# Kernel tuning notes

Hardware: AMD Instinct MI355X
Metric: run time of the kernel (lower is better)

## Reference

```python
import jax, jax.numpy as jnp
import numpy as np

B, S, H, F, E, K = 2, 2048, 1024, 2048, 8, 2  # batch, seq, hidden, ffn, experts, top_k


def setup_inputs() -> dict:
    key = jax.random.key(0)
    k1, k2, k3, k4 = jax.random.split(key, 4)
    s = lambda n: 1.0 / np.sqrt(n)
    return {
        "x": jax.random.normal(k1, (B, S, H), jnp.float32),
        "w_router": jax.random.normal(k2, (H, E), jnp.float32) * s(H),
        "w_in": jax.random.normal(k3, (E, H, 2 * F), jnp.float32) * s(H),   # GLU: 2*ffn
        "w_out": jax.random.normal(k4, (E, F, H), jnp.float32) * s(F),
        "bias": jnp.zeros((H,), jnp.float32),
    }


def reference(x, w_router, w_in, w_out, bias):
    Bq, Sq, Hq = x.shape
    T = Bq * Sq
    xf = x.reshape(T, Hq)

    # --- TopKGating ---
    logits = xf @ w_router                       # [T, E]
    top_vals, top_idx = jax.lax.top_k(logits, K)  # [T, K]
    gates = jax.nn.softmax(top_vals, axis=-1)    # softmax over selected logits

    # JetMoE-style aux loss: switch loss + 0.1 * z-loss
    probs = jax.nn.softmax(logits, axis=-1)
    p = probs.sum(0); p = p / p.sum()
    freq = jnp.sum(jax.nn.one_hot(top_idx, E, dtype=logits.dtype), axis=(0, 1))
    f = freq / freq.sum()
    lsesq = jnp.sum(jax.nn.logsumexp(logits, axis=-1) ** 2)
    loss = E * jnp.sum(p * f) + 0.1 * lsesq / T

    # --- dispatch: one row per (token, selected expert) pair, token-major ---
    eid = top_idx.reshape(-1)                    # [T*K] expert id per row
    g = gates.reshape(-1)                        # [T*K] gate per row
    tok = jnp.repeat(jnp.arange(T), K)           # [T*K] source token per row
    xr = jnp.repeat(xf, K, axis=0)               # [T*K, H]

    # --- grouped expert GEMMs (masked per-expert; math-equivalent to grouped GEMM) ---
    out_rows = jnp.zeros((T * K, Hq), x.dtype)
    for e in range(E):
        sel = (eid == e).astype(x.dtype)[:, None]
        h = (xr * sel) @ w_in[e]                 # [T*K, 2F]
        a, gv = jnp.split(h, 2, axis=-1)
        h = jax.nn.silu(a) * gv                  # GLU
        out_rows = out_rows + sel * (h @ w_out[e])

    # --- combine: scale by gates, scatter-add back to tokens ---
    out_rows = out_rows * g[:, None]
    y = jax.ops.segment_sum(out_rows, tok, num_segments=T)
    y = y.reshape(Bq, Sq, Hq) + bias
    return y, loss
```

## Files before the change

kernel.cpp:

```cpp
#include <hip/hip_runtime.h>
#include <hip/hip_bf16.h>
#include <math.h>

#define T_TOK 4096
#define HDIM  1024
#define FDIM  2048
#define EDIM  8
#define KSEL  2
#define TKROW 8192
#define N2F   4096
#define MAX_SLOTS 72

typedef __attribute__((ext_vector_type(8))) short short8;
typedef __attribute__((ext_vector_type(4))) float f32x4;

__device__ __forceinline__ unsigned short f32_to_bf16(float f) {
  unsigned int u = __float_as_uint(f);
  u += 0x7FFFu + ((u >> 16) & 1u);
  return (unsigned short)(u >> 16);
}

__device__ __forceinline__ void gload16(const void* g, void* l) {
  __builtin_amdgcn_global_load_lds(
      (const __attribute__((address_space(1))) unsigned int*)g,
      (__attribute__((address_space(3))) unsigned int*)l, 16, 0, 0);
}


__global__ void conv_x_kernel(const float* __restrict__ x,
                              unsigned short* __restrict__ xb, int n) {
  int i = (blockIdx.x * blockDim.x + threadIdx.x) * 4;
  if (i < n) {
    float4 v = *(const float4*)(x + i);
    ushort4 o;
    o.x = f32_to_bf16(v.x); o.y = f32_to_bf16(v.y);
    o.z = f32_to_bf16(v.z); o.w = f32_to_bf16(v.w);
    *(ushort4*)(xb + i) = o;
  }
}

__global__ void transpose_conv_kernel(const float* __restrict__ in,
                                      unsigned short* __restrict__ out,
                                      int R, int C) {
  __shared__ float tile[64][65];
  long base = (long)blockIdx.z * (long)R * (long)C;
  int c0 = blockIdx.x * 64, r0 = blockIdx.y * 64;
  int tx = threadIdx.x & 63;
  int ty = threadIdx.x >> 6;
  #pragma unroll
  for (int j = 0; j < 64; j += 4) {
    int r = r0 + ty + j;
    tile[ty + j][tx] = in[base + (long)r * C + c0 + tx];
  }
  __syncthreads();
  #pragma unroll
  for (int j = 0; j < 64; j += 4) {
    int oc = ty + j;
    out[base + (long)(c0 + oc) * R + r0 + tx] = f32_to_bf16(tile[tx][oc]);
  }
}

__global__ void router_kernel(const float* __restrict__ x,
                              const float* __restrict__ wr,
                              int* __restrict__ eid, float* __restrict__ tgate,
                              float* __restrict__ p_sum,
                              float* __restrict__ lse2_sum,
                              int* __restrict__ counts) {
  __shared__ float s_p[EDIM];
  __shared__ float s_lse2;
  __shared__ int s_cnt[EDIM];
  if (threadIdx.x < EDIM) { s_p[threadIdx.x] = 0.f; s_cnt[threadIdx.x] = 0; }
  if (threadIdx.x == 0) s_lse2 = 0.f;
  __syncthreads();

  int wave = threadIdx.x >> 6;
  int lane = threadIdx.x & 63;

  for (int it = 0; it < 4; ++it) {
    int t = (blockIdx.x * 4 + wave) + it * 1024;
    float acc[EDIM];
    #pragma unroll
    for (int e = 0; e < EDIM; e++) acc[e] = 0.f;
    const float* xr = x + (long)t * HDIM;
    for (int h = lane; h < HDIM; h += 64) {
      float xv = xr[h];
      const float* w = wr + h * EDIM;
      #pragma unroll
      for (int e = 0; e < EDIM; e++) acc[e] += xv * w[e];
    }
    #pragma unroll
    for (int e = 0; e < EDIM; e++) {
      float v = acc[e];
      for (int off = 32; off > 0; off >>= 1) v += __shfl_down(v, off);
      acc[e] = v;
    }
    if (lane == 0) {
      float m = acc[0];
      #pragma unroll
      for (int e = 1; e < EDIM; e++) m = fmaxf(m, acc[e]);
      float ex[EDIM]; float se = 0.f;
      #pragma unroll
      for (int e = 0; e < EDIM; e++) { ex[e] = __expf(acc[e] - m); se += ex[e]; }
      float lse = m + __logf(se);
      atomicAdd(&s_lse2, lse * lse);
      float inv = 1.f / se;
      #pragma unroll
      for (int e = 0; e < EDIM; e++) atomicAdd(&s_p[e], ex[e] * inv);
      int i1 = 0;
      #pragma unroll
      for (int e = 1; e < EDIM; e++) if (acc[e] > acc[i1]) i1 = e;
      int i2 = (i1 == 0) ? 1 : 0;
      #pragma unroll
      for (int e = 0; e < EDIM; e++) if (e != i1 && acc[e] > acc[i2]) i2 = e;
      float g1 = 1.f / (1.f + __expf(acc[i2] - acc[i1]));
      eid[t * 2] = i1; eid[t * 2 + 1] = i2;
      tgate[t * 2] = g1; tgate[t * 2 + 1] = 1.f - g1;
      atomicAdd(&s_cnt[i1], 1); atomicAdd(&s_cnt[i2], 1);
    }
  }
  __syncthreads();
  if (threadIdx.x < EDIM) {
    atomicAdd(&p_sum[threadIdx.x], s_p[threadIdx.x]);
    atomicAdd(&counts[threadIdx.x], s_cnt[threadIdx.x]);
  }
  if (threadIdx.x == 0) atomicAdd(lse2_sum, s_lse2);
}

__global__ void scan_kernel(const int* __restrict__ counts,
                            int* __restrict__ offsets, int* __restrict__ slot_e,
                            int* __restrict__ slot_m0, int* __restrict__ slot_rows,
                            int* __restrict__ n_slots, int* __restrict__ cursors) {
  int off = 0, s = 0;
  for (int e = 0; e < EDIM; e++) {
    offsets[e] = off;
    cursors[e] = 0;
    int c = counts[e];
    for (int m0 = 0; m0 < c; m0 += 128) {
      slot_e[s] = e; slot_m0[s] = off + m0;
      slot_rows[s] = min(128, c - m0); s++;
    }
    off += c;
  }
  *n_slots = s;
}

__global__ void scatter_kernel(const int* __restrict__ eid,
                               const float* __restrict__ tgate,
                               const int* __restrict__ offsets,
                               int* __restrict__ cursors,
                               int* __restrict__ btok, float* __restrict__ bgate,
                               int* __restrict__ tpos) {
  __shared__ int lcnt[EDIM];
  __shared__ int lbase[EDIM];
  int tid = threadIdx.x;
  if (tid < EDIM) lcnt[tid] = 0;
  __syncthreads();
  int t = blockIdx.x * 256 + tid;
  int e0 = eid[t * 2], e1 = eid[t * 2 + 1];
  int p0 = atomicAdd(&lcnt[e0], 1);
  int p1 = atomicAdd(&lcnt[e1], 1);
  __syncthreads();
  if (tid < EDIM) lbase[tid] = atomicAdd(&cursors[tid], lcnt[tid]);
  __syncthreads();
  int r0 = offsets[e0] + lbase[e0] + p0;
  int r1 = offsets[e1] + lbase[e1] + p1;
  btok[r0] = t; bgate[r0] = tgate[t * 2];     tpos[t * 2] = r0;
  btok[r1] = t; bgate[r1] = tgate[t * 2 + 1]; tpos[t * 2 + 1] = r1;
}

__global__ __launch_bounds__(256) void gemm1_kernel(
    const unsigned short* __restrict__ xb,
    const unsigned short* __restrict__ w_inT,
    const int* __restrict__ btok,
    const int* __restrict__ slot_e, const int* __restrict__ slot_m0,
    const int* __restrict__ slot_rows, const int* __restrict__ n_slots,
    unsigned short* __restrict__ glu)
{
  int bx = blockIdx.x;
  int slot = (bx & 7) * 9 + (bx >> 3);
  if (slot >= *n_slots) return;
  int e = slot_e[slot], r0 = slot_m0[slot], nrows = slot_rows[slot];
  int by = blockIdx.y;

  __shared__ unsigned short lA[128 * 64];
  __shared__ unsigned short lB[128 * 64];

  int tid = threadIdx.x;
  int lane = tid & 63, wv = tid >> 6;
  int wr = wv >> 1, wc = wv & 1;
  int lm = lane & 15, lq = lane >> 4, l7 = lane & 7;

  int srow = tid >> 3, skc = tid & 7;
  const unsigned short* asrc[4];
  const unsigned short* bsrc[4];
  #pragma unroll
  for (int i = 0; i < 4; ++i) {
    int row = srow + i * 32;
    int swz = (skc ^ (row & 7)) * 8;
    int ar = min(row, nrows - 1);
    int tok = btok[r0 + ar];
    asrc[i] = xb + (long)tok * HDIM + swz;
    int group = row >> 5, within = row & 31;
    int bcol = by * 64 + (group >> 1) * 32 + within + ((group & 1) ? FDIM : 0);
    bsrc[i] = w_inT + ((long)e * N2F + bcol) * HDIM + swz;
  }
  unsigned short* adst = lA + tid * 8;
  unsigned short* bdst = lB + tid * 8;

  f32x4 acc[4][4];
  #pragma unroll
  for (int mf = 0; mf < 4; ++mf)
    #pragma unroll
    for (int nf = 0; nf < 4; ++nf) acc[mf][nf] = (f32x4){0.f, 0.f, 0.f, 0.f};

  for (int k0 = 0; k0 < HDIM; k0 += 64) {
    #pragma unroll
    for (int i = 0; i < 4; ++i) {
      gload16(asrc[i] + k0, adst + i * 2048);
      gload16(bsrc[i] + k0, bdst + i * 2048);
    }
    __syncthreads();
    #pragma unroll
    for (int ks = 0; ks < 2; ++ks) {
      short8 a[4], b[4];
      #pragma unroll
      for (int mf = 0; mf < 4; ++mf) {
        int row = wr * 64 + mf * 16 + lm;
        a[mf] = *(const short8*)&lA[row * 64 + (((ks * 4 + lq) ^ l7) * 8)];
      }
      #pragma unroll
      for (int nf = 0; nf < 4; ++nf) {
        int n = wc * 64 + nf * 16 + lm;
        b[nf] = *(const short8*)&lB[n * 64 + (((ks * 4 + lq) ^ l7) * 8)];
      }
      #pragma unroll
      for (int mf = 0; mf < 4; ++mf)
        #pragma unroll
        for (int nf = 0; nf < 4; ++nf)
          acc[mf][nf] = __builtin_amdgcn_mfma_f32_16x16x32_bf16(a[mf], b[nf], acc[mf][nf], 0, 0, 0);
    }
    __syncthreads();
  }

  #pragma unroll
  for (int mf = 0; mf < 4; ++mf) {
    #pragma unroll
    for (int r = 0; r < 4; ++r) {
      int row = wr * 64 + mf * 16 + lq * 4 + r;
      if (row < nrows) {
        #pragma unroll
        for (int nf = 0; nf < 2; ++nf) {
          float a = acc[mf][nf][r];
          float g = acc[mf][nf + 2][r];
          float val = (a / (1.f + __expf(-a))) * g;
          glu[(long)(r0 + row) * FDIM + by * 64 + wc * 32 + nf * 16 + lm] = f32_to_bf16(val);
        }
      }
    }
  }
}

__global__ __launch_bounds__(256) void gemm2_kernel(
    const unsigned short* __restrict__ glu,
    const unsigned short* __restrict__ w_outT,
    const float* __restrict__ bgate,
    const int* __restrict__ slot_e, const int* __restrict__ slot_m0,
    const int* __restrict__ slot_rows, const int* __restrict__ n_slots,
    float* __restrict__ orows)
{
  int bx = blockIdx.x;
  int slot = (bx & 7) * 9 + (bx >> 3);
  if (slot >= *n_slots) return;
  int e = slot_e[slot], r0 = slot_m0[slot], nrows = slot_rows[slot];
  int c0 = blockIdx.y * 128;

  __shared__ unsigned short lA[128 * 64];
  __shared__ unsigned short lB[128 * 64];

  int tid = threadIdx.x;
  int lane = tid & 63, wv = tid >> 6;
  int wr = wv >> 1, wc = wv & 1;
  int lm = lane & 15, lq = lane >> 4, l7 = lane & 7;

  int srow = tid >> 3, skc = tid & 7;
  const unsigned short* asrc[4];
  const unsigned short* bsrc[4];
  #pragma unroll
  for (int i = 0; i < 4; ++i) {
    int row = srow + i * 32;
    int swz = (skc ^ (row & 7)) * 8;
    int ar = min(row, nrows - 1);
    asrc[i] = glu + (long)(r0 + ar) * FDIM + swz;
    bsrc[i] = w_outT + ((long)e * HDIM + c0 + row) * FDIM + swz;
  }
  unsigned short* adst = lA + tid * 8;
  unsigned short* bdst = lB + tid * 8;

  f32x4 acc[4][4];
  #pragma unroll
  for (int mf = 0; mf < 4; ++mf)
    #pragma unroll
    for (int nf = 0; nf < 4; ++nf) acc[mf][nf] = (f32x4){0.f, 0.f, 0.f, 0.f};

  for (int k0 = 0; k0 < FDIM; k0 += 64) {
    #pragma unroll
    for (int i = 0; i < 4; ++i) {
      gload16(asrc[i] + k0, adst + i * 2048);
      gload16(bsrc[i] + k0, bdst + i * 2048);
    }
    __syncthreads();
    #pragma unroll
    for (int ks = 0; ks < 2; ++ks) {
      short8 a[4], b[4];
      #pragma unroll
      for (int mf = 0; mf < 4; ++mf) {
        int row = wr * 64 + mf * 16 + lm;
        a[mf] = *(const short8*)&lA[row * 64 + (((ks * 4 + lq) ^ l7) * 8)];
      }
      #pragma unroll
      for (int nf = 0; nf < 4; ++nf) {
        int n = wc * 64 + nf * 16 + lm;
        b[nf] = *(const short8*)&lB[n * 64 + (((ks * 4 + lq) ^ l7) * 8)];
      }
      #pragma unroll
      for (int mf = 0; mf < 4; ++mf)
        #pragma unroll
        for (int nf = 0; nf < 4; ++nf)
          acc[mf][nf] = __builtin_amdgcn_mfma_f32_16x16x32_bf16(a[mf], b[nf], acc[mf][nf], 0, 0, 0);
    }
    __syncthreads();
  }

  #pragma unroll
  for (int mf = 0; mf < 4; ++mf) {
    #pragma unroll
    for (int r = 0; r < 4; ++r) {
      int row = wr * 64 + mf * 16 + lq * 4 + r;
      if (row < nrows) {
        float g = bgate[r0 + row];
        #pragma unroll
        for (int nf = 0; nf < 4; ++nf) {
          orows[(long)(r0 + row) * HDIM + c0 + wc * 64 + nf * 16 + lm] = acc[mf][nf][r] * g;
        }
      }
    }
  }
}

__global__ void combine_kernel(const float* __restrict__ orows,
                               const int* __restrict__ tpos,
                               const float* __restrict__ bias,
                               float* __restrict__ y) {
  int i = blockIdx.x * 256 + threadIdx.x;
  int t = i >> 8;
  int h = (i & 255) * 4;
  int p0 = tpos[t * 2], p1 = tpos[t * 2 + 1];
  float4 a = *(const float4*)(orows + (long)p0 * HDIM + h);
  float4 b = *(const float4*)(orows + (long)p1 * HDIM + h);
  float4 bv = *(const float4*)(bias + h);
  float4 o;
  o.x = a.x + b.x + bv.x; o.y = a.y + b.y + bv.y;
  o.z = a.z + b.z + bv.z; o.w = a.w + b.w + bv.w;
  *(float4*)(y + (long)t * HDIM + h) = o;
}

__global__ void finalize_kernel(const float* __restrict__ p_sum,
                                const float* __restrict__ lse2,
                                const int* __restrict__ counts,
                                float* __restrict__ loss_out) {
  float P = 0.f;
  for (int e = 0; e < EDIM; e++) P += p_sum[e];
  float dot = 0.f;
  for (int e = 0; e < EDIM; e++)
    dot += (p_sum[e] / P) * ((float)counts[e] / (float)TKROW);
  *loss_out = (float)EDIM * dot + 0.1f * (*lse2) / (float)T_TOK;
}

extern "C" void kernel_launch(void* const* d_in, const int* in_sizes, int n_in,
                              void* d_out, int out_size, void* d_ws, size_t ws_size,
                              hipStream_t stream) {
  const float* x        = (const float*)d_in[0];
  const float* w_router = (const float*)d_in[1];
  const float* w_in     = (const float*)d_in[2];
  const float* w_out    = (const float*)d_in[3];
  const float* bias     = (const float*)d_in[4];
  float* y = (float*)d_out;

  char* ws = (char*)d_ws;
  size_t o = 0;
  auto alloc = [&](size_t bytes) { size_t r = o; o = (o + bytes + 255) & ~(size_t)255; return r; };
  size_t o_meta    = alloc(256);
  size_t o_offsets = alloc(EDIM * 4);
  size_t o_slot_e  = alloc(MAX_SLOTS * 4);
  size_t o_slot_m0 = alloc(MAX_SLOTS * 4);
  size_t o_slot_nr = alloc(MAX_SLOTS * 4);
  size_t o_eid     = alloc((size_t)T_TOK * 2 * 4);
  size_t o_tgate   = alloc((size_t)T_TOK * 2 * 4);
  size_t o_tpos    = alloc((size_t)T_TOK * 2 * 4);
  size_t o_btok    = alloc((size_t)TKROW * 4);
  size_t o_bgate   = alloc((size_t)TKROW * 4);
  size_t o_xb      = alloc((size_t)T_TOK * HDIM * 2);
  size_t o_winT    = alloc((size_t)EDIM * N2F * HDIM * 2);
  size_t o_woutT   = alloc((size_t)EDIM * HDIM * FDIM * 2);
  size_t o_glu     = alloc((size_t)TKROW * FDIM * 2);
  size_t o_orows   = o_winT;
  (void)ws_size;

  float* p_sum   = (float*)(ws + o_meta);
  float* lse2    = (float*)(ws + o_meta + 32);
  int*   counts  = (int*)(ws + o_meta + 64);
  int*   cursors = (int*)(ws + o_meta + 96);
  int*   n_slots = (int*)(ws + o_meta + 128);
  int*   offsets = (int*)(ws + o_offsets);
  int*   slot_e  = (int*)(ws + o_slot_e);
  int*   slot_m0 = (int*)(ws + o_slot_m0);
  int*   slot_nr = (int*)(ws + o_slot_nr);
  int*   eid     = (int*)(ws + o_eid);
  float* tgate   = (float*)(ws + o_tgate);
  int*   tpos    = (int*)(ws + o_tpos);
  int*   btok    = (int*)(ws + o_btok);
  float* bgate   = (float*)(ws + o_bgate);
  unsigned short* xb    = (unsigned short*)(ws + o_xb);
  unsigned short* winT  = (unsigned short*)(ws + o_winT);
  unsigned short* woutT = (unsigned short*)(ws + o_woutT);
  unsigned short* glu   = (unsigned short*)(ws + o_glu);
  float* orows = (float*)(ws + o_orows);

  hipMemsetAsync(ws, 0, 256, stream);

  conv_x_kernel<<<dim3((T_TOK * HDIM) / 1024), dim3(256), 0, stream>>>(
      x, xb, T_TOK * HDIM);
  transpose_conv_kernel<<<dim3(N2F / 64, HDIM / 64, EDIM), dim3(256), 0, stream>>>(
      w_in, winT, HDIM, N2F);
  transpose_conv_kernel<<<dim3(HDIM / 64, FDIM / 64, EDIM), dim3(256), 0, stream>>>(
      w_out, woutT, FDIM, HDIM);

  router_kernel<<<dim3(256), dim3(256), 0, stream>>>(
      x, w_router, eid, tgate, p_sum, lse2, counts);
  scan_kernel<<<dim3(1), dim3(1), 0, stream>>>(
      counts, offsets, slot_e, slot_m0, slot_nr, n_slots, cursors);
  scatter_kernel<<<dim3(T_TOK / 256), dim3(256), 0, stream>>>(
      eid, tgate, offsets, cursors, btok, bgate, tpos);

  gemm1_kernel<<<dim3(MAX_SLOTS, FDIM / 64), dim3(256), 0, stream>>>(
      xb, winT, btok, slot_e, slot_m0, slot_nr, n_slots, glu);
  gemm2_kernel<<<dim3(MAX_SLOTS, HDIM / 128), dim3(256), 0, stream>>>(
      glu, woutT, bgate, slot_e, slot_m0, slot_nr, n_slots, orows);

  combine_kernel<<<dim3((T_TOK * HDIM) / 1024), dim3(256), 0, stream>>>(
      orows, tpos, bias, y);
  finalize_kernel<<<dim3(1), dim3(1), 0, stream>>>(
      p_sum, lse2, counts, y + (size_t)T_TOK * HDIM);
}
```

Measured before the change: 523.9 us.

## Double-buffer LDS tiles in expert GEMMs and vectorize transpose stores

Both grouped expert GEMM kernels now use two LDS buffers per operand. The next K-tile's global-to-LDS loads are issued before the MFMA work on the current tile, which removes one barrier per iteration and overlaps memory latency with compute. This doubles LDS use per block (64KB) and may lower occupancy. The weight transpose/convert kernel also writes packed bf16 pairs instead of single bf16 values.

```diff
diff --git a/kernel.cpp b/kernel.cpp
--- a/kernel.cpp
+++ b/kernel.cpp
@@ -53,10 +53,15 @@
     tile[ty + j][tx] = in[base + (long)r * C + c0 + tx];
   }
   __syncthreads();
-  #pragma unroll
-  for (int j = 0; j < 64; j += 4) {
-    int oc = ty + j;
-    out[base + (long)(c0 + oc) * R + r0 + tx] = f32_to_bf16(tile[tx][oc]);
+  int ow = threadIdx.x & 31;
+  int ocg = threadIdx.x >> 5;
+  #pragma unroll
+  for (int j = 0; j < 64; j += 8) {
+    int oc = ocg + j;
+    ushort2 o;
+    o.x = f32_to_bf16(tile[2 * ow][oc]);
+    o.y = f32_to_bf16(tile[2 * ow + 1][oc]);
+    *(ushort2*)(out + base + (long)(c0 + oc) * R + r0 + 2 * ow) = o;
   }
 }
 
@@ -182,8 +187,8 @@
   int e = slot_e[slot], r0 = slot_m0[slot], nrows = slot_rows[slot];
   int by = blockIdx.y;
 
-  __shared__ unsigned short lA[128 * 64];
-  __shared__ unsigned short lB[128 * 64];
+  __shared__ unsigned short lA[2][128 * 64];
+  __shared__ unsigned short lB[2][128 * 64];
 
   int tid = threadIdx.x;
   int lane = tid & 63, wv = tid >> 6;
@@ -204,8 +209,6 @@
     int bcol = by * 64 + (group >> 1) * 32 + within + ((group & 1) ? FDIM : 0);
     bsrc[i] = w_inT + ((long)e * N2F + bcol) * HDIM + swz;
   }
-  unsigned short* adst = lA + tid * 8;
-  unsigned short* bdst = lB + tid * 8;
 
   f32x4 acc[4][4];
   #pragma unroll
@@ -213,25 +216,35 @@
     #pragma unroll
     for (int nf = 0; nf < 4; ++nf) acc[mf][nf] = (f32x4){0.f, 0.f, 0.f, 0.f};
 
-  for (int k0 = 0; k0 < HDIM; k0 += 64) {
-    #pragma unroll
-    for (int i = 0; i < 4; ++i) {
-      gload16(asrc[i] + k0, adst + i * 2048);
-      gload16(bsrc[i] + k0, bdst + i * 2048);
-    }
+  #pragma unroll
+  for (int i = 0; i < 4; ++i) {
+    gload16(asrc[i], &lA[0][tid * 8 + i * 2048]);
+    gload16(bsrc[i], &lB[0][tid * 8 + i * 2048]);
+  }
+  int cur = 0;
+  for (int it = 0; it < HDIM / 64; ++it) {
     __syncthreads();
+    if (it + 1 < HDIM / 64) {
+      int k0 = (it + 1) * 64;
+      int nxt = cur ^ 1;
+      #pragma unroll
+      for (int i = 0; i < 4; ++i) {
+        gload16(asrc[i] + k0, &lA[nxt][tid * 8 + i * 2048]);
+        gload16(bsrc[i] + k0, &lB[nxt][tid * 8 + i * 2048]);
+      }
+    }
     #pragma unroll
     for (int ks = 0; ks < 2; ++ks) {
       short8 a[4], b[4];
       #pragma unroll
       for (int mf = 0; mf < 4; ++mf) {
         int row = wr * 64 + mf * 16 + lm;
-        a[mf] = *(const short8*)&lA[row * 64 + (((ks * 4 + lq) ^ l7) * 8)];
+        a[mf] = *(const short8*)&lA[cur][row * 64 + (((ks * 4 + lq) ^ l7) * 8)];
       }
       #pragma unroll
       for (int nf = 0; nf < 4; ++nf) {
         int n = wc * 64 + nf * 16 + lm;
-        b[nf] = *(const short8*)&lB[n * 64 + (((ks * 4 + lq) ^ l7) * 8)];
+        b[nf] = *(const short8*)&lB[cur][n * 64 + (((ks * 4 + lq) ^ l7) * 8)];
       }
       #pragma unroll
       for (int mf = 0; mf < 4; ++mf)
@@ -239,7 +252,7 @@
         for (int nf = 0; nf < 4; ++nf)
           acc[mf][nf] = __builtin_amdgcn_mfma_f32_16x16x32_bf16(a[mf], b[nf], acc[mf][nf], 0, 0, 0);
     }
-    __syncthreads();
+    cur ^= 1;
   }
 
   #pragma unroll
@@ -274,8 +287,8 @@
   int e = slot_e[slot], r0 = slot_m0[slot], nrows = slot_rows[slot];
   int c0 = blockIdx.y * 128;
 
-  __shared__ unsigned short lA[128 * 64];
-  __shared__ unsigned short lB[128 * 64];
+  __shared__ unsigned short lA[2][128 * 64];
+  __shared__ unsigned short lB[2][128 * 64];
 
   int tid = threadIdx.x;
   int lane = tid & 63, wv = tid >> 6;
@@ -293,8 +306,6 @@
     asrc[i] = glu + (long)(r0 + ar) * FDIM + swz;
     bsrc[i] = w_outT + ((long)e * HDIM + c0 + row) * FDIM + swz;
   }
-  unsigned short* adst = lA + tid * 8;
-  unsigned short* bdst = lB + tid * 8;
 
   f32x4 acc[4][4];
   #pragma unroll
@@ -302,25 +313,35 @@
     #pragma unroll
     for (int nf = 0; nf < 4; ++nf) acc[mf][nf] = (f32x4){0.f, 0.f, 0.f, 0.f};
 
-  for (int k0 = 0; k0 < FDIM; k0 += 64) {
-    #pragma unroll
-    for (int i = 0; i < 4; ++i) {
-      gload16(asrc[i] + k0, adst + i * 2048);
-      gload16(bsrc[i] + k0, bdst + i * 2048);
-    }
+  #pragma unroll
+  for (int i = 0; i < 4; ++i) {
+    gload16(asrc[i], &lA[0][tid * 8 + i * 2048]);
+    gload16(bsrc[i], &lB[0][tid * 8 + i * 2048]);
+  }
+  int cur = 0;
+  for (int it = 0; it < FDIM / 64; ++it) {
     __syncthreads();
+    if (it + 1 < FDIM / 64) {
+      int k0 = (it + 1) * 64;
+      int nxt = cur ^ 1;
+      #pragma unroll
+      for (int i = 0; i < 4; ++i) {
+        gload16(asrc[i] + k0, &lA[nxt][tid * 8 + i * 2048]);
+        gload16(bsrc[i] + k0, &lB[nxt][tid * 8 + i * 2048]);
+      }
+    }
     #pragma unroll
     for (int ks = 0; ks < 2; ++ks) {
       short8 a[4], b[4];
       #pragma unroll
       for (int mf = 0; mf < 4; ++mf) {
         int row = wr * 64 + mf * 16 + lm;
-        a[mf] = *(const short8*)&lA[row * 64 + (((ks * 4 + lq) ^ l7) * 8)];
+        a[mf] = *(const short8*)&lA[cur][row * 64 + (((ks * 4 + lq) ^ l7) * 8)];
       }
       #pragma unroll
       for (int nf = 0; nf < 4; ++nf) {
         int n = wc * 64 + nf * 16 + lm;
-        b[nf] = *(const short8*)&lB[n * 64 + (((ks * 4 + lq) ^ l7) * 8)];
+        b[nf] = *(const short8*)&lB[cur][n * 64 + (((ks * 4 + lq) ^ l7) * 8)];
       }
       #pragma unroll
       for (int mf = 0; mf < 4; ++mf)
@@ -328,7 +349,7 @@
         for (int nf = 0; nf < 4; ++nf)
           acc[mf][nf] = __builtin_amdgcn_mfma_f32_16x16x32_bf16(a[mf], b[nf], acc[mf][nf], 0, 0, 0);
     }
-    __syncthreads();
+    cur ^= 1;
   }
 
   #pragma unroll
```

After: 586.1 us. +11.9%, slower.

## Fuse x bf16 conversion into router, widen gemm1 N tile, vectorize transpose stores

Applied to the files above, without the earlier changes.

Drops the standalone x-to-bf16 conversion kernel and does the conversion inside the router kernel, which already reads x, saving one full pass over the activations and one launch. The router inner loop now reads float4 vectors. The GLU GEMM tile grows from 64 to 128 output columns per block (256 B rows covering both halves), so each A tile loaded into LDS is reused across twice as many columns, at the cost of more accumulator registers and LDS per block and half as many blocks. The weight transpose kernel now writes packed pairs of bf16 values instead of single 16-bit stores.

```diff
diff --git a/kernel.cpp b/kernel.cpp
--- a/kernel.cpp
+++ b/kernel.cpp
@@ -27,18 +27,6 @@
 }
 
 
-__global__ void conv_x_kernel(const float* __restrict__ x,
-                              unsigned short* __restrict__ xb, int n) {
-  int i = (blockIdx.x * blockDim.x + threadIdx.x) * 4;
-  if (i < n) {
-    float4 v = *(const float4*)(x + i);
-    ushort4 o;
-    o.x = f32_to_bf16(v.x); o.y = f32_to_bf16(v.y);
-    o.z = f32_to_bf16(v.z); o.w = f32_to_bf16(v.w);
-    *(ushort4*)(xb + i) = o;
-  }
-}
-
 __global__ void transpose_conv_kernel(const float* __restrict__ in,
                                       unsigned short* __restrict__ out,
                                       int R, int C) {
@@ -53,15 +41,21 @@
     tile[ty + j][tx] = in[base + (long)r * C + c0 + tx];
   }
   __syncthreads();
-  #pragma unroll
-  for (int j = 0; j < 64; j += 4) {
-    int oc = ty + j;
-    out[base + (long)(c0 + oc) * R + r0 + tx] = f32_to_bf16(tile[tx][oc]);
+  int ow = threadIdx.x & 31;
+  int ocg = threadIdx.x >> 5;
+  #pragma unroll
+  for (int j = 0; j < 64; j += 8) {
+    int oc = ocg + j;
+    ushort2 o;
+    o.x = f32_to_bf16(tile[2 * ow][oc]);
+    o.y = f32_to_bf16(tile[2 * ow + 1][oc]);
+    *(ushort2*)(out + base + (long)(c0 + oc) * R + r0 + 2 * ow) = o;
   }
 }
 
 __global__ void router_kernel(const float* __restrict__ x,
                               const float* __restrict__ wr,
+                              unsigned short* __restrict__ xbout,
                               int* __restrict__ eid, float* __restrict__ tgate,
                               float* __restrict__ p_sum,
                               float* __restrict__ lse2_sum,
@@ -82,11 +76,20 @@
     #pragma unroll
     for (int e = 0; e < EDIM; e++) acc[e] = 0.f;
     const float* xr = x + (long)t * HDIM;
-    for (int h = lane; h < HDIM; h += 64) {
-      float xv = xr[h];
-      const float* w = wr + h * EDIM;
-      #pragma unroll
-      for (int e = 0; e < EDIM; e++) acc[e] += xv * w[e];
+    unsigned short* xo = xbout + (long)t * HDIM;
+    #pragma unroll
+    for (int c = 0; c < 4; ++c) {
+      int h0 = lane * 4 + c * 256;
+      float4 v = *(const float4*)(xr + h0);
+      ushort4 o;
+      o.x = f32_to_bf16(v.x); o.y = f32_to_bf16(v.y);
+      o.z = f32_to_bf16(v.z); o.w = f32_to_bf16(v.w);
+      *(ushort4*)(xo + h0) = o;
+      const float* w0 = wr + (long)h0 * EDIM;
+      #pragma unroll
+      for (int e = 0; e < EDIM; e++)
+        acc[e] += v.x * w0[e] + v.y * w0[EDIM + e] +
+                  v.z * w0[2 * EDIM + e] + v.w * w0[3 * EDIM + e];
     }
     #pragma unroll
     for (int e = 0; e < EDIM; e++) {
@@ -183,7 +186,7 @@
   int by = blockIdx.y;
 
   __shared__ unsigned short lA[128 * 64];
-  __shared__ unsigned short lB[128 * 64];
+  __shared__ unsigned short lB[256 * 64];
 
   int tid = threadIdx.x;
   int lane = tid & 63, wv = tid >> 6;
@@ -192,7 +195,7 @@
 
   int srow = tid >> 3, skc = tid & 7;
   const unsigned short* asrc[4];
-  const unsigned short* bsrc[4];
+  const unsigned short* bsrc[8];
   #pragma unroll
   for (int i = 0; i < 4; ++i) {
     int row = srow + i * 32;
@@ -200,44 +203,45 @@
     int ar = min(row, nrows - 1);
     int tok = btok[r0 + ar];
     asrc[i] = xb + (long)tok * HDIM + swz;
-    int group = row >> 5, within = row & 31;
-    int bcol = by * 64 + (group >> 1) * 32 + within + ((group & 1) ? FDIM : 0);
+  }
+  #pragma unroll
+  for (int i = 0; i < 8; ++i) {
+    int row = srow + i * 32;
+    int swz = (skc ^ (row & 7)) * 8;
+    int w = row >> 7, r = row & 127;
+    int bcol = (r < 64) ? (by * 128 + w * 64 + r)
+                        : (FDIM + by * 128 + w * 64 + (r - 64));
     bsrc[i] = w_inT + ((long)e * N2F + bcol) * HDIM + swz;
   }
-  unsigned short* adst = lA + tid * 8;
-  unsigned short* bdst = lB + tid * 8;
-
-  f32x4 acc[4][4];
+
+  f32x4 acc[4][8];
   #pragma unroll
   for (int mf = 0; mf < 4; ++mf)
     #pragma unroll
-    for (int nf = 0; nf < 4; ++nf) acc[mf][nf] = (f32x4){0.f, 0.f, 0.f, 0.f};
+    for (int nf = 0; nf < 8; ++nf) acc[mf][nf] = (f32x4){0.f, 0.f, 0.f, 0.f};
 
   for (int k0 = 0; k0 < HDIM; k0 += 64) {
     #pragma unroll
-    for (int i = 0; i < 4; ++i) {
-      gload16(asrc[i] + k0, adst + i * 2048);
-      gload16(bsrc[i] + k0, bdst + i * 2048);
-    }
+    for (int i = 0; i < 4; ++i) gload16(asrc[i] + k0, &lA[tid * 8 + i * 2048]);
+    #pragma unroll
+    for (int i = 0; i < 8; ++i) gload16(bsrc[i] + k0, &lB[tid * 8 + i * 2048]);
     __syncthreads();
     #pragma unroll
     for (int ks = 0; ks < 2; ++ks) {
-      short8 a[4], b[4];
+      short8 a[4];
       #pragma unroll
       for (int mf = 0; mf < 4; ++mf) {
         int row = wr * 64 + mf * 16 + lm;
         a[mf] = *(const short8*)&lA[row * 64 + (((ks * 4 + lq) ^ l7) * 8)];
       }
       #pragma unroll
-      for (int nf = 0; nf < 4; ++nf) {
-        int n = wc * 64 + nf * 16 + lm;
-        b[nf] = *(const short8*)&lB[n * 64 + (((ks * 4 + lq) ^ l7) * 8)];
-      }
-      #pragma unroll
-      for (int mf = 0; mf < 4; ++mf)
+      for (int nf = 0; nf < 8; ++nf) {
+        int n = wc * 128 + nf * 16 + lm;
+        short8 b = *(const short8*)&lB[n * 64 + (((ks * 4 + lq) ^ l7) * 8)];
         #pragma unroll
-        for (int nf = 0; nf < 4; ++nf)
-          acc[mf][nf] = __builtin_amdgcn_mfma_f32_16x16x32_bf16(a[mf], b[nf], acc[mf][nf], 0, 0, 0);
+        for (int mf = 0; mf < 4; ++mf)
+          acc[mf][nf] = __builtin_amdgcn_mfma_f32_16x16x32_bf16(a[mf], b, acc[mf][nf], 0, 0, 0);
+      }
     }
     __syncthreads();
   }
@@ -249,11 +253,11 @@
       int row = wr * 64 + mf * 16 + lq * 4 + r;
       if (row < nrows) {
         #pragma unroll
-        for (int nf = 0; nf < 2; ++nf) {
+        for (int nf = 0; nf < 4; ++nf) {
           float a = acc[mf][nf][r];
-          float g = acc[mf][nf + 2][r];
+          float g = acc[mf][nf + 4][r];
           float val = (a / (1.f + __expf(-a))) * g;
-          glu[(long)(r0 + row) * FDIM + by * 64 + wc * 32 + nf * 16 + lm] = f32_to_bf16(val);
+          glu[(long)(r0 + row) * FDIM + by * 128 + wc * 64 + nf * 16 + lm] = f32_to_bf16(val);
         }
       }
     }
@@ -293,8 +297,6 @@
     asrc[i] = glu + (long)(r0 + ar) * FDIM + swz;
     bsrc[i] = w_outT + ((long)e * HDIM + c0 + row) * FDIM + swz;
   }
-  unsigned short* adst = lA + tid * 8;
-  unsigned short* bdst = lB + tid * 8;
 
   f32x4 acc[4][4];
   #pragma unroll
@@ -305,8 +307,8 @@
   for (int k0 = 0; k0 < FDIM; k0 += 64) {
     #pragma unroll
     for (int i = 0; i < 4; ++i) {
-      gload16(asrc[i] + k0, adst + i * 2048);
-      gload16(bsrc[i] + k0, bdst + i * 2048);
+      gload16(asrc[i] + k0, &lA[tid * 8 + i * 2048]);
+      gload16(bsrc[i] + k0, &lB[tid * 8 + i * 2048]);
     }
     __syncthreads();
     #pragma unroll
@@ -428,21 +430,19 @@
 
   hipMemsetAsync(ws, 0, 256, stream);
 
-  conv_x_kernel<<<dim3((T_TOK * HDIM) / 1024), dim3(256), 0, stream>>>(
-      x, xb, T_TOK * HDIM);
   transpose_conv_kernel<<<dim3(N2F / 64, HDIM / 64, EDIM), dim3(256), 0, stream>>>(
       w_in, winT, HDIM, N2F);
   transpose_conv_kernel<<<dim3(HDIM / 64, FDIM / 64, EDIM), dim3(256), 0, stream>>>(
       w_out, woutT, FDIM, HDIM);
 
   router_kernel<<<dim3(256), dim3(256), 0, stream>>>(
-      x, w_router, eid, tgate, p_sum, lse2, counts);
+      x, w_router, xb, eid, tgate, p_sum, lse2, counts);
   scan_kernel<<<dim3(1), dim3(1), 0, stream>>>(
       counts, offsets, slot_e, slot_m0, slot_nr, n_slots, cursors);
   scatter_kernel<<<dim3(T_TOK / 256), dim3(256), 0, stream>>>(
       eid, tgate, offsets, cursors, btok, bgate, tpos);
 
-  gemm1_kernel<<<dim3(MAX_SLOTS, FDIM / 64), dim3(256), 0, stream>>>(
+  gemm1_kernel<<<dim3(MAX_SLOTS, FDIM / 128), dim3(256), 0, stream>>>(
       xb, winT, btok, slot_e, slot_m0, slot_nr, n_slots, glu);
   gemm2_kernel<<<dim3(MAX_SLOTS, HDIM / 128), dim3(256), 0, stream>>>(
       glu, woutT, bgate, slot_e, slot_m0, slot_nr, n_slots, orows);
```

New measurement: 559.8 us. 1.07x slower.
